# Performance work log

Hardware: AMD Instinct MI355X
Metric: run time of the kernel (lower is better)

Reference implementation:

```python
import jax, jax.numpy as jnp
import numpy as np

B, N, D, H, DFF = 8, 1024, 1024, 16, 4096
HD = D // H

def _xavier(key, shape):
    fan_in, fan_out = shape[1], shape[0]
    limit = float(np.sqrt(6.0 / (fan_in + fan_out)))
    return jax.random.uniform(key, shape, jnp.float32, -limit, limit)

def setup_inputs() -> dict:
    key = jax.random.key(0)
    ks = jax.random.split(key, 8)
    return {
        'src':    jax.random.normal(ks[0], (B, N, D), jnp.float32),
        'wqkv':   _xavier(ks[1], (3 * D, D)),
        'bqkv':   jnp.zeros((3 * D,), jnp.float32),
        'wo':     _xavier(ks[2], (D, D)),
        'bo':     jnp.zeros((D,), jnp.float32),
        'g1':     jnp.ones((D,), jnp.float32),
        'b1':     jnp.zeros((D,), jnp.float32),
        'g2':     jnp.ones((D,), jnp.float32),
        'b2':     jnp.zeros((D,), jnp.float32),
        'w_gate': _xavier(ks[3], (DFF, D)),
        'b_gate': jnp.zeros((DFF,), jnp.float32),
        'w_up':   _xavier(ks[4], (DFF, D)),
        'b_up':   jnp.zeros((DFF,), jnp.float32),
        'w_down': _xavier(ks[5], (D, DFF)),
        'b_down': jnp.zeros((D,), jnp.float32),
    }

def _layernorm(x, g, b, eps=1e-5):
    mu = jnp.mean(x, axis=-1, keepdims=True)
    var = jnp.var(x, axis=-1, keepdims=True)
    return (x - mu) * jax.lax.rsqrt(var + eps) * g + b

def _alibi_slopes(heads):
    # m_h = 2^(-8h/H), h = 1..H
    return jnp.asarray(2.0 ** (-8.0 * np.arange(1, heads + 1) / heads), jnp.float32)

def _attention(x, wqkv, bqkv, wo, bo):
    qkv = x @ wqkv.T + bqkv                      # [B,N,3D]
    q, k, v = jnp.split(qkv, 3, axis=-1)
    def heads(t):
        return t.reshape(B, N, H, HD).transpose(0, 2, 1, 3)  # [B,H,N,D]
    q, k, v = heads(q), heads(k), heads(v)
    # ALiBi bias: -slope * |i - j|, broadcast over batch
    pos = jnp.arange(N, dtype=jnp.float32)
    dist = jnp.abs(pos[:, None] - pos[None, :])  # [N,N]
    bias = -_alibi_slopes(H)[:, None, None] * dist  # [H,N,N]
    scale = 1.0 / np.sqrt(HD)
    scores = jnp.einsum('bhnd,bhmd->bhnm', q, k) * scale + bias[None]
    attn = jax.nn.softmax(scores, axis=-1)
    out = jnp.einsum('bhnm,bhmd->bhnd', attn, v)
    out = out.transpose(0, 2, 1, 3).reshape(B, N, D)
    return out @ wo.T + bo

def _swiglu(x, w_gate, b_gate, w_up, b_up, w_down, b_down):
    gate = jax.nn.silu(x @ w_gate.T + b_gate)
    up = x @ w_up.T + b_up
    return (gate * up) @ w_down.T + b_down

def reference(src, wqkv, bqkv, wo, bo, g1, b1, g2, b2,
              w_gate, b_gate, w_up, b_up, w_down, b_down):
    x = src + _attention(_layernorm(src, g1, b1), wqkv, bqkv, wo, bo)
    x = x + _swiglu(_layernorm(x, g2, b2), w_gate, b_gate, w_up, b_up, w_down, b_down)
    return x
```

## Files before the change

### kernel.cpp

```cpp
#include <hip/hip_runtime.h>

#define Bz 8
#define Nz 1024
#define Dz 1024
#define Hz 16
#define HDz 64
#define DFFz 4096

typedef __attribute__((ext_vector_type(8))) __bf16 bh8;
typedef __attribute__((ext_vector_type(4))) __bf16 bh4;
typedef __attribute__((ext_vector_type(4))) float f4;

#define GLOAD16(gp, lp) __builtin_amdgcn_global_load_lds( \
    (__attribute__((address_space(1))) void*)(gp), \
    (__attribute__((address_space(3))) void*)(lp), 16, 0, 0)

__global__ __launch_bounds__(256) void cvt_k(const float* __restrict__ in,
                                             __bf16* __restrict__ out, int n4) {
    int i = blockIdx.x * 256 + threadIdx.x;
    if (i < n4) {
        float4 v = ((const float4*)in)[i];
        bh4 o;
        o[0] = (__bf16)v.x; o[1] = (__bf16)v.y; o[2] = (__bf16)v.z; o[3] = (__bf16)v.w;
        ((bh4*)out)[i] = o;
    }
}

__global__ __launch_bounds__(256) void ln_k(const float* __restrict__ x,
                                            const float* __restrict__ g,
                                            const float* __restrict__ bb,
                                            __bf16* __restrict__ out) {
    const int row = blockIdx.x, t = threadIdx.x;
    const float4 v = ((const float4*)(x + (size_t)row * Dz))[t];
    float s = v.x + v.y + v.z + v.w;
    float s2 = v.x * v.x + v.y * v.y + v.z * v.z + v.w * v.w;
#pragma unroll
    for (int off = 32; off > 0; off >>= 1) {
        s += __shfl_down(s, off);
        s2 += __shfl_down(s2, off);
    }
    __shared__ float ps[4], ps2[4];
    if ((t & 63) == 0) { ps[t >> 6] = s; ps2[t >> 6] = s2; }
    __syncthreads();
    float ts = 0.f, ts2 = 0.f;
#pragma unroll
    for (int i = 0; i < 4; i++) { ts += ps[i]; ts2 += ps2[i]; }
    const float mean = ts * (1.f / Dz);
    const float var = ts2 * (1.f / Dz) - mean * mean;
    const float inv = rsqrtf(var + 1e-5f);
    const float4 gv = ((const float4*)g)[t];
    const float4 bv = ((const float4*)bb)[t];
    bh4 o;
    o[0] = (__bf16)((v.x - mean) * inv * gv.x + bv.x);
    o[1] = (__bf16)((v.y - mean) * inv * gv.y + bv.y);
    o[2] = (__bf16)((v.z - mean) * inv * gv.z + bv.z);
    o[3] = (__bf16)((v.w - mean) * inv * gv.w + bv.w);
    *(bh4*)&out[(size_t)row * Dz + t * 4] = o;
}

template <int EPI>
__global__ __launch_bounds__(256) void gemm128(
    const __bf16* __restrict__ A, const __bf16* __restrict__ W,
    const float* __restrict__ bias, void* __restrict__ outp,
    const float* __restrict__ addf, const __bf16* __restrict__ upb,
    int M, int N, int K) {
    __shared__ __align__(16) __bf16 lsA[2 * 128 * 32];
    __shared__ __align__(16) __bf16 lsB[2 * 128 * 32];
    const int t = threadIdx.x;
    const int w = t >> 6, l = t & 63;
    const int brow = blockIdx.y, bcol = blockIdx.x;

    const __bf16* Ag = A + (size_t)(brow * 128 + (t >> 2)) * K + (t & 3) * 8;
    const __bf16* Wg = W + (size_t)(bcol * 128 + (t >> 2)) * K + (t & 3) * 8;

    const f4 zf = {0.f, 0.f, 0.f, 0.f};
    f4 acc[4][4];
#pragma unroll
    for (int m = 0; m < 4; m++)
#pragma unroll
        for (int n = 0; n < 4; n++) acc[m][n] = zf;

    const int lo = l & 15, hi = l >> 4;
    const int rowA = (w >> 1) * 64 + lo;
    const int colB = (w & 1) * 64 + lo;
    const int kk = hi * 8;

#define STAGE(P, KOFF) do { \
        GLOAD16(Ag + (KOFF), lsA + (P) * 4096 + w * 512); \
        GLOAD16(Ag + (size_t)64 * K + (KOFF), lsA + (P) * 4096 + w * 512 + 64 * 32); \
        GLOAD16(Wg + (KOFF), lsB + (P) * 4096 + w * 512); \
        GLOAD16(Wg + (size_t)64 * K + (KOFF), lsB + (P) * 4096 + w * 512 + 64 * 32); \
    } while (0)

#define COMPUTE(P) do { \
        const __bf16* la = lsA + (P) * 4096; \
        const __bf16* lb = lsB + (P) * 4096; \
        bh8 af[4], bfv[4]; \
        _Pragma("unroll") \
        for (int m = 0; m < 4; m++) af[m] = *(const bh8*)&la[(rowA + m * 16) * 32 + kk]; \
        _Pragma("unroll") \
        for (int n = 0; n < 4; n++) bfv[n] = *(const bh8*)&lb[(colB + n * 16) * 32 + kk]; \
        _Pragma("unroll") \
        for (int m = 0; m < 4; m++) \
            _Pragma("unroll") \
            for (int n = 0; n < 4; n++) \
                acc[m][n] = __builtin_amdgcn_mfma_f32_16x16x32_bf16(af[m], bfv[n], acc[m][n], 0, 0, 0); \
    } while (0)

    const int nt = K >> 5;
    int cur = 0;
    STAGE(0, 0);
    __syncthreads();
    for (int kt = 0; kt < nt - 1; ++kt) {
        STAGE(cur ^ 1, (kt + 1) * 32);
        COMPUTE(cur);
        __syncthreads();
        cur ^= 1;
    }
    COMPUTE(cur);
#undef STAGE
#undef COMPUTE

    const int gr0 = brow * 128 + (w >> 1) * 64;
    const int gc0 = bcol * 128 + (w & 1) * 64;
#pragma unroll
    for (int m = 0; m < 4; m++)
#pragma unroll
        for (int n = 0; n < 4; n++) {
            const int col = gc0 + n * 16 + lo;
            const float bv = bias[col];
#pragma unroll
            for (int j = 0; j < 4; j++) {
                const int row = gr0 + m * 16 + hi * 4 + j;
                const size_t idx = (size_t)row * N + col;
                const float v = acc[m][n][j] + bv;
                if (EPI == 0) {
                    ((__bf16*)outp)[idx] = (__bf16)v;
                } else if (EPI == 1 || EPI == 2) {
                    ((float*)outp)[idx] = addf[idx] + v;
                } else {
                    const float u = (float)upb[idx];
                    const float sv = v / (1.f + __expf(-v));
                    ((__bf16*)outp)[idx] = (__bf16)(sv * u);
                }
            }
        }
}

__global__ __launch_bounds__(256) void attn_k(const __bf16* __restrict__ qkv,
                                              __bf16* __restrict__ out) {
    const int t = threadIdx.x, w = t >> 6, l = t & 63;
    const int qt = blockIdx.x, h = blockIdx.y, b = blockIdx.z;
    const int qbase = qt * 64;
    const int lo = l & 15, hi = l >> 4;
    const float slope = exp2f(-0.5f * (float)(h + 1));

    const size_t base = (size_t)b * Nz * 3072 + h * 64;
    const __bf16* qp = qkv + base;
    const __bf16* kp = qkv + base + 1024;
    const __bf16* vp = qkv + base + 2048;

    __shared__ __align__(16) __bf16 lsK[64 * 64];
    __shared__ __align__(16) __bf16 lsVt[64 * 72];
    __shared__ __align__(16) __bf16 lsP[4 * 16 * 64];

    const int myq = qbase + w * 16 + lo;
    const bh8 qf0 = *(const bh8*)(qp + (size_t)myq * 3072 + hi * 8);
    const bh8 qf1 = *(const bh8*)(qp + (size_t)myq * 3072 + 32 + hi * 8);

    const f4 zf = {0.f, 0.f, 0.f, 0.f};
    float m_run[4], l_run[4];
    f4 oacc[4];
#pragma unroll
    for (int jj = 0; jj < 4; jj++) { m_run[jj] = -1e30f; l_run[jj] = 0.f; }
#pragma unroll
    for (int n = 0; n < 4; n++) oacc[n] = zf;

    const int jr = t >> 2, d0 = (t & 3) * 16;

    for (int j0 = 0; j0 < Nz; j0 += 64) {
        __syncthreads();
        {
            const __bf16* krow = kp + (size_t)(j0 + jr) * 3072 + d0;
            const int sw = (jr & 7) * 8;
            *(bh8*)&lsK[jr * 64 + (d0 ^ sw)] = *(const bh8*)krow;
            *(bh8*)&lsK[jr * 64 + ((d0 + 8) ^ sw)] = *(const bh8*)(krow + 8);
        }
        {
            const int d = t & 63;
            bh8 t0, t1;
#pragma unroll
            for (int jj = 0; jj < 8; jj++) t0[jj] = vp[(size_t)(j0 + w * 16 + jj) * 3072 + d];
#pragma unroll
            for (int jj = 0; jj < 8; jj++) t1[jj] = vp[(size_t)(j0 + w * 16 + 8 + jj) * 3072 + d];
            *(bh8*)&lsVt[d * 72 + w * 16] = t0;
            *(bh8*)&lsVt[d * 72 + w * 16 + 8] = t1;
        }
        __syncthreads();

        float vals[4][4];
#pragma unroll
        for (int c = 0; c < 4; c++) {
            const int krw = c * 16 + lo;
            const int swr = (krw & 7);
            const bh8 kf0 = *(const bh8*)&lsK[krw * 64 + 8 * (hi ^ swr)];
            const bh8 kf1 = *(const bh8*)&lsK[krw * 64 + 8 * ((4 + hi) ^ swr)];
            f4 s = zf;
            s = __builtin_amdgcn_mfma_f32_16x16x32_bf16(qf0, kf0, s, 0, 0, 0);
            s = __builtin_amdgcn_mfma_f32_16x16x32_bf16(qf1, kf1, s, 0, 0, 0);
            const int gj = j0 + c * 16 + lo;
#pragma unroll
            for (int jj = 0; jj < 4; jj++) {
                const int gq = qbase + w * 16 + hi * 4 + jj;
                vals[c][jj] = s[jj] * 0.125f - slope * fabsf((float)(gq - gj));
            }
        }
        float mc[4];
#pragma unroll
        for (int jj = 0; jj < 4; jj++)
            mc[jj] = fmaxf(fmaxf(vals[0][jj], vals[1][jj]), fmaxf(vals[2][jj], vals[3][jj]));
#pragma unroll
        for (int off = 8; off > 0; off >>= 1)
#pragma unroll
            for (int jj = 0; jj < 4; jj++) mc[jj] = fmaxf(mc[jj], __shfl_xor(mc[jj], off));
        float corr[4], psum[4];
#pragma unroll
        for (int jj = 0; jj < 4; jj++) {
            const float mn = fmaxf(m_run[jj], mc[jj]);
            corr[jj] = __expf(m_run[jj] - mn);
            m_run[jj] = mn;
            psum[jj] = 0.f;
        }
#pragma unroll
        for (int c = 0; c < 4; c++)
#pragma unroll
            for (int jj = 0; jj < 4; jj++) {
                const float p = __expf(vals[c][jj] - m_run[jj]);
                vals[c][jj] = p;
                psum[jj] += p;
            }
#pragma unroll
        for (int off = 8; off > 0; off >>= 1)
#pragma unroll
            for (int jj = 0; jj < 4; jj++) psum[jj] += __shfl_xor(psum[jj], off);
#pragma unroll
        for (int jj = 0; jj < 4; jj++) l_run[jj] = l_run[jj] * corr[jj] + psum[jj];
#pragma unroll
        for (int n = 0; n < 4; n++)
#pragma unroll
            for (int jj = 0; jj < 4; jj++) oacc[n][jj] *= corr[jj];

#pragma unroll
        for (int c = 0; c < 4; c++)
#pragma unroll
            for (int jj = 0; jj < 4; jj++) {
                const int q = hi * 4 + jj;
                lsP[w * 1024 + q * 64 + ((c * 16 + lo) ^ ((q & 7) * 8))] = (__bf16)vals[c][jj];
            }

        const int psw = (lo & 7);
        const bh8 pa0 = *(const bh8*)&lsP[w * 1024 + lo * 64 + 8 * (hi ^ psw)];
        const bh8 pa1 = *(const bh8*)&lsP[w * 1024 + lo * 64 + 8 * ((4 + hi) ^ psw)];

#pragma unroll
        for (int n = 0; n < 4; n++) {
            const bh8 vf0 = *(const bh8*)&lsVt[(n * 16 + lo) * 72 + hi * 8];
            const bh8 vf1 = *(const bh8*)&lsVt[(n * 16 + lo) * 72 + 32 + hi * 8];
            oacc[n] = __builtin_amdgcn_mfma_f32_16x16x32_bf16(pa0, vf0, oacc[n], 0, 0, 0);
            oacc[n] = __builtin_amdgcn_mfma_f32_16x16x32_bf16(pa1, vf1, oacc[n], 0, 0, 0);
        }
    }

#pragma unroll
    for (int n = 0; n < 4; n++)
#pragma unroll
        for (int jj = 0; jj < 4; jj++) {
            const int gq = qbase + w * 16 + hi * 4 + jj;
            const int d = n * 16 + lo;
            out[((size_t)b * Nz + gq) * Dz + h * 64 + d] = (__bf16)(oacc[n][jj] / l_run[jj]);
        }
}

extern "C" void kernel_launch(void* const* d_in, const int* in_sizes, int n_in,
                              void* d_out, int out_size, void* d_ws, size_t ws_size,
                              hipStream_t stream) {
    const float* src  = (const float*)d_in[0];
    const float* wqkv = (const float*)d_in[1];
    const float* bqkv = (const float*)d_in[2];
    const float* wo   = (const float*)d_in[3];
    const float* bo   = (const float*)d_in[4];
    const float* g1   = (const float*)d_in[5];
    const float* b1   = (const float*)d_in[6];
    const float* g2   = (const float*)d_in[7];
    const float* b2   = (const float*)d_in[8];
    const float* wg   = (const float*)d_in[9];
    const float* bg   = (const float*)d_in[10];
    const float* wu   = (const float*)d_in[11];
    const float* bu   = (const float*)d_in[12];
    const float* wd   = (const float*)d_in[13];
    const float* bd   = (const float*)d_in[14];
    float* out = (float*)d_out;

    __bf16* wqkv_b = (__bf16*)d_ws;
    __bf16* wo_b   = wqkv_b + (size_t)3072 * 1024;
    __bf16* wg_b   = wo_b + (size_t)1024 * 1024;
    __bf16* wu_b   = wg_b + (size_t)4096 * 1024;
    __bf16* wd_b   = wu_b + (size_t)4096 * 1024;
    __bf16* lnbuf  = wd_b + (size_t)1024 * 4096;
    __bf16* qkv    = lnbuf + (size_t)8192 * 1024;
    __bf16* attno  = qkv + (size_t)8192 * 3072;
    float*  x1     = (float*)(attno + (size_t)8192 * 1024);
    __bf16* hb     = qkv;

    cvt_k<<<3072, 256, 0, stream>>>(wqkv, wqkv_b, 3072 * 1024 / 4);
    cvt_k<<<1024, 256, 0, stream>>>(wo, wo_b, 1024 * 1024 / 4);
    cvt_k<<<4096, 256, 0, stream>>>(wg, wg_b, 4096 * 1024 / 4);
    cvt_k<<<4096, 256, 0, stream>>>(wu, wu_b, 4096 * 1024 / 4);
    cvt_k<<<4096, 256, 0, stream>>>(wd, wd_b, 1024 * 4096 / 4);

    ln_k<<<8192, 256, 0, stream>>>(src, g1, b1, lnbuf);
    gemm128<0><<<dim3(3072 / 128, 8192 / 128), 256, 0, stream>>>(
        lnbuf, wqkv_b, bqkv, qkv, nullptr, nullptr, 8192, 3072, 1024);
    attn_k<<<dim3(16, 16, 8), 256, 0, stream>>>(qkv, attno);
    gemm128<1><<<dim3(1024 / 128, 8192 / 128), 256, 0, stream>>>(
        attno, wo_b, bo, x1, src, nullptr, 8192, 1024, 1024);

    ln_k<<<8192, 256, 0, stream>>>(x1, g2, b2, lnbuf);
    gemm128<0><<<dim3(4096 / 128, 8192 / 128), 256, 0, stream>>>(
        lnbuf, wu_b, bu, hb, nullptr, nullptr, 8192, 4096, 1024);
    gemm128<3><<<dim3(4096 / 128, 8192 / 128), 256, 0, stream>>>(
        lnbuf, wg_b, bg, hb, nullptr, hb, 8192, 4096, 1024);
    gemm128<2><<<dim3(1024 / 128, 8192 / 128), 256, 0, stream>>>(
        hb, wd_b, bd, out, x1, nullptr, 8192, 1024, 4096);
}
```

Baseline: 726.7 us.

## Replace 128x128 GEMM with 256xBN tiles, triple-buffered LDS and swizzle

The GEMM kernel moves from 128x128 tiles with 256 threads to 256-row by 128/256-column tiles with 512 threads (8 waves, 8xNB MFMA per wave). This raises data reuse per LDS load and lowers global traffic. It also adds a 3-stage LDS pipeline with explicit vmcnt waits and raw barriers, an XOR swizzle on LDS columns to avoid bank conflicts, and s_setprio around the MFMA block. In exchange it uses more registers and LDS per block, which may limit occupancy. Smaller grids for the N=1024 GEMMs (256 blocks) may underfill the GPU.

Result: slower. 762.2 us (+4.9%).

```diff
diff --git a/kernel.cpp b/kernel.cpp
--- a/kernel.cpp
+++ b/kernel.cpp
@@ -58,75 +58,89 @@
     *(bh4*)&out[(size_t)row * Dz + t * 4] = o;
 }
 
-template <int EPI>
-__global__ __launch_bounds__(256) void gemm128(
+template <int EPI, int BN>
+__global__ __launch_bounds__(512, 2) void gemm256(
     const __bf16* __restrict__ A, const __bf16* __restrict__ W,
     const float* __restrict__ bias, void* __restrict__ outp,
     const float* __restrict__ addf, const __bf16* __restrict__ upb,
     int M, int N, int K) {
-    __shared__ __align__(16) __bf16 lsA[2 * 128 * 32];
-    __shared__ __align__(16) __bf16 lsB[2 * 128 * 32];
+    constexpr int NB = BN / 64;
+    constexpr int ASZ = 256 * 32;
+    constexpr int BSZ = BN * 32;
+    constexpr int LPT = 2 + BN / 128;
+    __shared__ __align__(16) __bf16 lsA[3 * ASZ];
+    __shared__ __align__(16) __bf16 lsB[3 * BSZ];
     const int t = threadIdx.x;
     const int w = t >> 6, l = t & 63;
+    const int lo = l & 15, hi = l >> 4;
+    const int wr = w >> 2, wc = w & 3;
     const int brow = blockIdx.y, bcol = blockIdx.x;
 
-    const __bf16* Ag = A + (size_t)(brow * 128 + (t >> 2)) * K + (t & 3) * 8;
-    const __bf16* Wg = W + (size_t)(bcol * 128 + (t >> 2)) * K + (t & 3) * 8;
+    const int sr = t >> 2;
+    const int sc = (t & 3) ^ ((sr >> 1) & 3);
+    const __bf16* Ag = A + (size_t)(brow * 256 + sr) * K + sc * 8;
+    const __bf16* Wg = W + (size_t)(bcol * BN + sr) * K + sc * 8;
 
     const f4 zf = {0.f, 0.f, 0.f, 0.f};
-    f4 acc[4][4];
-#pragma unroll
-    for (int m = 0; m < 4; m++)
-#pragma unroll
-        for (int n = 0; n < 4; n++) acc[m][n] = zf;
-
-    const int lo = l & 15, hi = l >> 4;
-    const int rowA = (w >> 1) * 64 + lo;
-    const int colB = (w & 1) * 64 + lo;
-    const int kk = hi * 8;
-
-#define STAGE(P, KOFF) do { \
-        GLOAD16(Ag + (KOFF), lsA + (P) * 4096 + w * 512); \
-        GLOAD16(Ag + (size_t)64 * K + (KOFF), lsA + (P) * 4096 + w * 512 + 64 * 32); \
-        GLOAD16(Wg + (KOFF), lsB + (P) * 4096 + w * 512); \
-        GLOAD16(Wg + (size_t)64 * K + (KOFF), lsB + (P) * 4096 + w * 512 + 64 * 32); \
+    f4 acc[8][NB];
+#pragma unroll
+    for (int m = 0; m < 8; m++)
+#pragma unroll
+        for (int n = 0; n < NB; n++) acc[m][n] = zf;
+
+    const int sl8 = 8 * (hi ^ ((lo >> 1) & 3));
+
+#define STAGE(BUF, KT) do { \
+        const size_t ko = (size_t)(KT) * 32; \
+        GLOAD16(Ag + ko, lsA + (BUF) * ASZ + w * 512); \
+        GLOAD16(Ag + (size_t)128 * K + ko, lsA + (BUF) * ASZ + 4096 + w * 512); \
+        GLOAD16(Wg + ko, lsB + (BUF) * BSZ + w * 512); \
+        if (BN == 256) GLOAD16(Wg + (size_t)128 * K + ko, lsB + (BUF) * BSZ + 4096 + w * 512); \
     } while (0)
 
-#define COMPUTE(P) do { \
-        const __bf16* la = lsA + (P) * 4096; \
-        const __bf16* lb = lsB + (P) * 4096; \
-        bh8 af[4], bfv[4]; \
+#define COMPUTE(BUF) do { \
+        const __bf16* la = lsA + (BUF) * ASZ; \
+        const __bf16* lb = lsB + (BUF) * BSZ; \
+        bh8 af[8], bfv[NB]; \
         _Pragma("unroll") \
-        for (int m = 0; m < 4; m++) af[m] = *(const bh8*)&la[(rowA + m * 16) * 32 + kk]; \
+        for (int m = 0; m < 8; m++) \
+            af[m] = *(const bh8*)&la[(wr * 128 + m * 16 + lo) * 32 + sl8]; \
         _Pragma("unroll") \
-        for (int n = 0; n < 4; n++) bfv[n] = *(const bh8*)&lb[(colB + n * 16) * 32 + kk]; \
+        for (int n = 0; n < NB; n++) \
+            bfv[n] = *(const bh8*)&lb[(wc * (BN / 4) + n * 16 + lo) * 32 + sl8]; \
+        __builtin_amdgcn_s_setprio(1); \
         _Pragma("unroll") \
-        for (int m = 0; m < 4; m++) \
+        for (int m = 0; m < 8; m++) \
             _Pragma("unroll") \
-            for (int n = 0; n < 4; n++) \
+            for (int n = 0; n < NB; n++) \
                 acc[m][n] = __builtin_amdgcn_mfma_f32_16x16x32_bf16(af[m], bfv[n], acc[m][n], 0, 0, 0); \
+        __builtin_amdgcn_s_setprio(0); \
     } while (0)
 
     const int nt = K >> 5;
-    int cur = 0;
     STAGE(0, 0);
-    __syncthreads();
-    for (int kt = 0; kt < nt - 1; ++kt) {
-        STAGE(cur ^ 1, (kt + 1) * 32);
-        COMPUTE(cur);
-        __syncthreads();
-        cur ^= 1;
+    STAGE(1, 1);
+    asm volatile("s_waitcnt vmcnt(%0)" :: "n"(LPT) : "memory");
+    __builtin_amdgcn_s_barrier();
+    for (int kt = 0; kt < nt - 2; ++kt) {
+        STAGE((kt + 2) % 3, kt + 2);
+        COMPUTE(kt % 3);
+        asm volatile("s_waitcnt vmcnt(%0) lgkmcnt(0)" :: "n"(LPT) : "memory");
+        __builtin_amdgcn_s_barrier();
     }
-    COMPUTE(cur);
+    COMPUTE((nt - 2) % 3);
+    asm volatile("s_waitcnt vmcnt(0) lgkmcnt(0)" ::: "memory");
+    __builtin_amdgcn_s_barrier();
+    COMPUTE((nt - 1) % 3);
 #undef STAGE
 #undef COMPUTE
 
-    const int gr0 = brow * 128 + (w >> 1) * 64;
-    const int gc0 = bcol * 128 + (w & 1) * 64;
-#pragma unroll
-    for (int m = 0; m < 4; m++)
-#pragma unroll
-        for (int n = 0; n < 4; n++) {
+    const int gr0 = brow * 256 + wr * 128;
+    const int gc0 = bcol * BN + wc * (BN / 4);
+#pragma unroll
+    for (int m = 0; m < 8; m++)
+#pragma unroll
+        for (int n = 0; n < NB; n++) {
             const int col = gc0 + n * 16 + lo;
             const float bv = bias[col];
 #pragma unroll
@@ -319,17 +333,17 @@
     cvt_k<<<4096, 256, 0, stream>>>(wd, wd_b, 1024 * 4096 / 4);
 
     ln_k<<<8192, 256, 0, stream>>>(src, g1, b1, lnbuf);
-    gemm128<0><<<dim3(3072 / 128, 8192 / 128), 256, 0, stream>>>(
+    gemm256<0, 128><<<dim3(3072 / 128, 8192 / 256), 512, 0, stream>>>(
         lnbuf, wqkv_b, bqkv, qkv, nullptr, nullptr, 8192, 3072, 1024);
     attn_k<<<dim3(16, 16, 8), 256, 0, stream>>>(qkv, attno);
-    gemm128<1><<<dim3(1024 / 128, 8192 / 128), 256, 0, stream>>>(
+    gemm256<1, 128><<<dim3(1024 / 128, 8192 / 256), 512, 0, stream>>>(
         attno, wo_b, bo, x1, src, nullptr, 8192, 1024, 1024);
 
     ln_k<<<8192, 256, 0, stream>>>(x1, g2, b2, lnbuf);
-    gemm128<0><<<dim3(4096 / 128, 8192 / 128), 256, 0, stream>>>(
+    gemm256<0, 256><<<dim3(4096 / 256, 8192 / 256), 512, 0, stream>>>(
         lnbuf, wu_b, bu, hb, nullptr, nullptr, 8192, 4096, 1024);
-    gemm128<3><<<dim3(4096 / 128, 8192 / 128), 256, 0, stream>>>(
+    gemm256<3, 256><<<dim3(4096 / 256, 8192 / 256), 512, 0, stream>>>(
         lnbuf, wg_b, bg, hb, nullptr, hb, 8192, 4096, 1024);
-    gemm128<2><<<dim3(1024 / 128, 8192 / 128), 256, 0, stream>>>(
+    gemm256<2, 128><<<dim3(1024 / 128, 8192 / 256), 512, 0, stream>>>(
         hb, wd_b, bd, out, x1, nullptr, 8192, 1024, 4096);
 }
```
